# Performance work log

Measured on AMD Instinct MI355X. Metric: run time of the kernel, lower is better.

The kernel has to match this reference:

```python
import jax, jax.numpy as jnp
import numpy as np

B, L, H, HEADS = 4, 256, 256, 4
D = H // HEADS
NEG = jnp.float32(-2.0**32 + 1)


def setup_inputs() -> dict:
    key = jax.random.key(0)
    ks = jax.random.split(key, 16)
    inp = {
        "queries": jax.random.normal(ks[0], (B, L, H), jnp.float32),
        "keys": jax.random.normal(ks[1], (B, L, H), jnp.float32),
        "values": jax.random.normal(ks[2], (B, L, H), jnp.float32),
        "time_matrix_K": jax.random.normal(ks[3], (B, L, L, H), jnp.float32),
        "time_matrix_V": jax.random.normal(ks[4], (B, L, L, H), jnp.float32),
        "abs_pos_K": jax.random.normal(ks[5], (B, L, H), jnp.float32),
        "abs_pos_V": jax.random.normal(ks[6], (B, L, H), jnp.float32),
        "time_mask": jax.random.randint(ks[7], (B, L), 0, 2) == 1,
        "future_time_mask": jnp.triu(jnp.ones((L, L), bool), k=1),
        # linear layer params (torch Linear: y = x @ W.T + b)
        "Wq": jax.random.normal(ks[8], (H, H), jnp.float32) / np.sqrt(H),
        "bq": jax.random.normal(ks[9], (H,), jnp.float32) * 0.01,
        "Wk": jax.random.normal(ks[10], (H, H), jnp.float32) / np.sqrt(H),
        "bk": jax.random.normal(ks[11], (H,), jnp.float32) * 0.01,
        "Wv": jax.random.normal(ks[12], (H, H), jnp.float32) / np.sqrt(H),
        "bv": jax.random.normal(ks[13], (H,), jnp.float32) * 0.01,
    }
    return inp


def _split_heads(x):  # [B,L,H] -> [h,B,L,d]
    b, l, _ = x.shape
    return x.reshape(b, l, HEADS, D).transpose(2, 0, 1, 3)


def _split_heads_rel(t):  # [B,L,L,H] -> [h,B,L,L,d]
    b, l, _, _ = t.shape
    return t.reshape(b, l, l, HEADS, D).transpose(3, 0, 1, 2, 4)


def reference(queries, keys, values, time_matrix_K, time_matrix_V,
              abs_pos_K, abs_pos_V, time_mask, future_time_mask,
              Wq, bq, Wk, bk, Wv, bv):
    Q = _split_heads(queries @ Wq.T + bq)   # [h,B,L,d]
    K = _split_heads(keys @ Wk.T + bk)
    V = _split_heads(values @ Wv.T + bv)
    tK = _split_heads_rel(time_matrix_K)    # [h,B,L,L,d]
    tV = _split_heads_rel(time_matrix_V)
    pK = _split_heads(abs_pos_K)            # [h,B,L,d]
    pV = _split_heads(abs_pos_V)

    scores = jnp.einsum("hbqd,hbkd->hbqk", Q, K)
    scores += jnp.einsum("hbqd,hbkd->hbqk", Q, pK)
    scores += jnp.einsum("hbqkd,hbqd->hbqk", tK, Q)
    scores = scores / jnp.sqrt(jnp.float32(D))

    mask = time_mask[None, :, :, None] | future_time_mask[None, None, :, :]
    scores = jnp.where(mask, NEG, scores)
    attn = jax.nn.softmax(scores, axis=-1)  # [h,B,L,L]  (dropout: eval mode)

    out = jnp.einsum("hbqk,hbkd->hbqd", attn, V)
    out += jnp.einsum("hbqk,hbkd->hbqd", attn, pV)
    out += jnp.einsum("hbqk,hbqkd->hbqd", attn, tV)
    # merge heads: [h,B,L,d] -> [B,L,H]
    return out.transpose(1, 2, 0, 3).reshape(B, L, H)
```

## Files before the change

kernel.cpp:

```cpp
#include <hip/hip_runtime.h>
#include <math.h>
#include <stdint.h>

#define LSEQ 256
#define HD 256

typedef float floatx4 __attribute__((ext_vector_type(4)));

__device__ __forceinline__ float dot4(float4 a, float4 b) {
    return a.x * b.x + a.y * b.y + a.z * b.z + a.w * b.w;
}
__device__ __forceinline__ float4 add4(float4 a, float4 b) {
    return make_float4(a.x + b.x, a.y + b.y, a.z + b.z, a.w + b.w);
}
__device__ __forceinline__ float4 ldnt4(const float* p) {
    floatx4 r = __builtin_nontemporal_load((const floatx4*)p);
    return make_float4(r.x, r.y, r.z, r.w);
}

__global__ __launch_bounds__(256) void proj_kernel(
    const float* __restrict__ queries, const float* __restrict__ keys,
    const float* __restrict__ values,
    const float* __restrict__ apK, const float* __restrict__ apV,
    const float* __restrict__ Wq, const float* __restrict__ bq,
    const float* __restrict__ Wk, const float* __restrict__ bk,
    const float* __restrict__ Wv, const float* __restrict__ bv,
    float* __restrict__ Qo, float* __restrict__ Ko, float* __restrict__ Vo)
{
    const int R = 4;
    int tid = threadIdx.x;
    int row0 = blockIdx.x * R;

    float aq[R] = {0.f, 0.f, 0.f, 0.f};
    float ak[R] = {0.f, 0.f, 0.f, 0.f};
    float av[R] = {0.f, 0.f, 0.f, 0.f};

    const float* wq = Wq + tid * HD;
    const float* wk = Wk + tid * HD;
    const float* wv = Wv + tid * HD;

    #pragma unroll 2
    for (int i = 0; i < HD; i += 4) {
        float4 wq4 = *(const float4*)(wq + i);
        float4 wk4 = *(const float4*)(wk + i);
        float4 wv4 = *(const float4*)(wv + i);
        #pragma unroll
        for (int r = 0; r < R; ++r) {
            float4 xq = *(const float4*)(queries + (row0 + r) * HD + i);
            float4 xk = *(const float4*)(keys    + (row0 + r) * HD + i);
            float4 xv = *(const float4*)(values  + (row0 + r) * HD + i);
            aq[r] += dot4(xq, wq4);
            ak[r] += dot4(xk, wk4);
            av[r] += dot4(xv, wv4);
        }
    }
    #pragma unroll
    for (int r = 0; r < R; ++r) {
        int idx = (row0 + r) * HD + tid;
        Qo[idx] = aq[r] + bq[tid];
        Ko[idx] = ak[r] + bk[tid] + apK[idx];
        Vo[idx] = av[r] + bv[tid] + apV[idx];
    }
}

__global__ __launch_bounds__(256) void vmean_kernel(
    const float* __restrict__ Veff, float* __restrict__ Vm)
{
    int b = blockIdx.x;
    int t = threadIdx.x;
    const float* Vb = Veff + b * (LSEQ * HD);
    float s = 0.f;
    #pragma unroll 4
    for (int k = 0; k < LSEQ; ++k)
        s += Vb[k * HD + t];
    Vm[b * HD + t] = s * (1.0f / 256.0f);
}

__global__ __launch_bounds__(512) void attn_kernel(
    const float* __restrict__ Q, const float* __restrict__ Keff,
    const float* __restrict__ Veff, const float* __restrict__ tK,
    const float* __restrict__ tV, const float* __restrict__ Vm,
    const int* __restrict__ tmask, float* __restrict__ out)
{
    __shared__ float sc[4][260];
    __shared__ float outp[8][256];

    int bid = blockIdx.x;
    int q = 255 - (bid >> 2);
    int b = bid & 3;
    int bq = (b << 8) | q;

    int tid = threadIdx.x;
    int w = tid >> 6;
    int lane = tid & 63;
    int head = lane >> 4;
    int le4 = lane * 4;

    bool masked = tmask[bq] != 0;

    const float* tVr = tV + (size_t)bq * (LSEQ * HD);
    float4 acc = make_float4(0.f, 0.f, 0.f, 0.f);

    if (masked) {
        int r0 = w * 32;
        #pragma unroll 1
        for (int k = r0; k < r0 + 32; k += 8) {
            float4 t0 = ldnt4(tVr + (k    ) * HD + le4);
            float4 t1 = ldnt4(tVr + (k + 1) * HD + le4);
            float4 t2 = ldnt4(tVr + (k + 2) * HD + le4);
            float4 t3 = ldnt4(tVr + (k + 3) * HD + le4);
            float4 t4 = ldnt4(tVr + (k + 4) * HD + le4);
            float4 t5 = ldnt4(tVr + (k + 5) * HD + le4);
            float4 t6 = ldnt4(tVr + (k + 6) * HD + le4);
            float4 t7 = ldnt4(tVr + (k + 7) * HD + le4);
            acc.x += ((t0.x + t1.x) + (t2.x + t3.x)) + ((t4.x + t5.x) + (t6.x + t7.x));
            acc.y += ((t0.y + t1.y) + (t2.y + t3.y)) + ((t4.y + t5.y) + (t6.y + t7.y));
            acc.z += ((t0.z + t1.z) + (t2.z + t3.z)) + ((t4.z + t5.z) + (t6.z + t7.z));
            acc.w += ((t0.w + t1.w) + (t2.w + t3.w)) + ((t4.w + t5.w) + (t6.w + t7.w));
        }
    } else {
        const float* tKr = tK + (size_t)bq * (LSEQ * HD);
        const float* Kb  = Keff + b * (LSEQ * HD);
        const float* Vb  = Veff + b * (LSEQ * HD);
        float4 q4 = *(const float4*)(Q + bq * HD + le4);

        int nk = q + 1;
        int run = (nk + 7) >> 3;
        int r0 = w * run;
        int rend = min(r0 + run, nk);

        int k = r0;
        for (; k + 3 < rend; k += 4) {
            float4 t0 = ldnt4(tKr + (k    ) * HD + le4);
            float4 t1 = ldnt4(tKr + (k + 1) * HD + le4);
            float4 t2 = ldnt4(tKr + (k + 2) * HD + le4);
            float4 t3 = ldnt4(tKr + (k + 3) * HD + le4);
            float4 c0 = *(const float4*)(Kb + (k    ) * HD + le4);
            float4 c1 = *(const float4*)(Kb + (k + 1) * HD + le4);
            float4 c2 = *(const float4*)(Kb + (k + 2) * HD + le4);
            float4 c3 = *(const float4*)(Kb + (k + 3) * HD + le4);
            float s0 = dot4(q4, add4(t0, c0));
            float s1 = dot4(q4, add4(t1, c1));
            float s2 = dot4(q4, add4(t2, c2));
            float s3 = dot4(q4, add4(t3, c3));
            #pragma unroll
            for (int off = 1; off <= 8; off <<= 1) {
                s0 += __shfl_xor(s0, off);
                s1 += __shfl_xor(s1, off);
                s2 += __shfl_xor(s2, off);
                s3 += __shfl_xor(s3, off);
            }
            if ((lane & 15) == 0) {
                sc[head][k    ] = s0 * 0.125f;
                sc[head][k + 1] = s1 * 0.125f;
                sc[head][k + 2] = s2 * 0.125f;
                sc[head][k + 3] = s3 * 0.125f;
            }
        }
        for (; k < rend; ++k) {
            float4 t0 = ldnt4(tKr + k * HD + le4);
            float4 c0 = *(const float4*)(Kb + k * HD + le4);
            float s0 = dot4(q4, add4(t0, c0));
            #pragma unroll
            for (int off = 1; off <= 8; off <<= 1)
                s0 += __shfl_xor(s0, off);
            if ((lane & 15) == 0) sc[head][k] = s0 * 0.125f;
        }
        __syncthreads();

        if (w < 4) {
            int k0 = lane * 4;
            float4 vv = *(const float4*)(&sc[w][k0]);
            float x0 = (k0 + 0 <= q) ? vv.x : -INFINITY;
            float x1 = (k0 + 1 <= q) ? vv.y : -INFINITY;
            float x2 = (k0 + 2 <= q) ? vv.z : -INFINITY;
            float x3 = (k0 + 3 <= q) ? vv.w : -INFINITY;
            float m = fmaxf(fmaxf(x0, x1), fmaxf(x2, x3));
            #pragma unroll
            for (int off = 32; off >= 1; off >>= 1)
                m = fmaxf(m, __shfl_xor(m, off));
            float e0 = __expf(x0 - m);
            float e1 = __expf(x1 - m);
            float e2 = __expf(x2 - m);
            float e3 = __expf(x3 - m);
            float ssum = e0 + e1 + e2 + e3;
            #pragma unroll
            for (int off = 32; off >= 1; off >>= 1)
                ssum += __shfl_xor(ssum, off);
            float inv = 1.0f / ssum;
            *(float4*)(&sc[w][k0]) = make_float4(e0 * inv, e1 * inv,
                                                 e2 * inv, e3 * inv);
        }
        __syncthreads();

        k = r0;
        for (; k + 3 < rend; k += 4) {
            float4 t0 = ldnt4(tVr + (k    ) * HD + le4);
            float4 t1 = ldnt4(tVr + (k + 1) * HD + le4);
            float4 t2 = ldnt4(tVr + (k + 2) * HD + le4);
            float4 t3 = ldnt4(tVr + (k + 3) * HD + le4);
            float4 v0 = *(const float4*)(Vb + (k    ) * HD + le4);
            float4 v1 = *(const float4*)(Vb + (k + 1) * HD + le4);
            float4 v2 = *(const float4*)(Vb + (k + 2) * HD + le4);
            float4 v3 = *(const float4*)(Vb + (k + 3) * HD + le4);
            float a0 = sc[head][k    ];
            float a1 = sc[head][k + 1];
            float a2 = sc[head][k + 2];
            float a3 = sc[head][k + 3];
            acc.x += a0 * (t0.x + v0.x) + a1 * (t1.x + v1.x)
                   + a2 * (t2.x + v2.x) + a3 * (t3.x + v3.x);
            acc.y += a0 * (t0.y + v0.y) + a1 * (t1.y + v1.y)
                   + a2 * (t2.y + v2.y) + a3 * (t3.y + v3.y);
            acc.z += a0 * (t0.z + v0.z) + a1 * (t1.z + v1.z)
                   + a2 * (t2.z + v2.z) + a3 * (t3.z + v3.z);
            acc.w += a0 * (t0.w + v0.w) + a1 * (t1.w + v1.w)
                   + a2 * (t2.w + v2.w) + a3 * (t3.w + v3.w);
        }
        for (; k < rend; ++k) {
            float4 t0 = ldnt4(tVr + k * HD + le4);
            float4 v0 = *(const float4*)(Vb + k * HD + le4);
            float a0 = sc[head][k];
            acc.x += a0 * (t0.x + v0.x);
            acc.y += a0 * (t0.y + v0.y);
            acc.z += a0 * (t0.z + v0.z);
            acc.w += a0 * (t0.w + v0.w);
        }
    }

    *(float4*)(&outp[w][le4]) = acc;
    __syncthreads();
    if (tid < 256) {
        float o = 0.f;
        #pragma unroll
        for (int p = 0; p < 8; ++p) o += outp[p][tid];
        if (masked) o = o * (1.0f / 256.0f) + Vm[b * HD + tid];
        out[(size_t)bq * HD + tid] = o;
    }
}

extern "C" void kernel_launch(void* const* d_in, const int* in_sizes, int n_in,
                              void* d_out, int out_size, void* d_ws, size_t ws_size,
                              hipStream_t stream) {
    const float* queries = (const float*)d_in[0];
    const float* keys    = (const float*)d_in[1];
    const float* values  = (const float*)d_in[2];
    const float* tK      = (const float*)d_in[3];
    const float* tV      = (const float*)d_in[4];
    const float* apK     = (const float*)d_in[5];
    const float* apV     = (const float*)d_in[6];
    const int*   tmask   = (const int*)d_in[7];
    const float* Wq = (const float*)d_in[9];
    const float* bq = (const float*)d_in[10];
    const float* Wk = (const float*)d_in[11];
    const float* bk = (const float*)d_in[12];
    const float* Wv = (const float*)d_in[13];
    const float* bv = (const float*)d_in[14];

    float* ws = (float*)d_ws;
    float* Qo = ws;
    float* Ko = ws + 262144;
    float* Vo = ws + 524288;
    float* Vm = ws + 786432;
    float* out = (float*)d_out;

    proj_kernel<<<256, 256, 0, stream>>>(queries, keys, values, apK, apV,
                                         Wq, bq, Wk, bk, Wv, bv, Qo, Ko, Vo);
    vmean_kernel<<<4, 256, 0, stream>>>(Vo, Vm);
    attn_kernel<<<1024, 512, 0, stream>>>(Qo, Ko, Vo, tK, tV, Vm, tmask, out);
}
```

Before: 103.5 us.

## Software-pipeline attention row loads with double-buffered 8-row register batches

Replaces the 4-row unrolled score and value loops with a macro-driven double-buffered pipeline that loads 8 rows into one register set while consuming the previous set. The K and tK streams are split into separate passes, with an extra shared-memory buffer for the K partial scores, and likewise V and tV are accumulated in separate passes. Launch bounds now request 2 blocks per CU. The goal is more loads in flight to hide HBM latency on the large tK/tV streams, at the cost of more registers, extra LDS traffic and more shuffle reductions.

```diff
diff --git a/kernel.cpp b/kernel.cpp
--- a/kernel.cpp
+++ b/kernel.cpp
@@ -10,13 +10,74 @@
 __device__ __forceinline__ float dot4(float4 a, float4 b) {
     return a.x * b.x + a.y * b.y + a.z * b.z + a.w * b.w;
 }
-__device__ __forceinline__ float4 add4(float4 a, float4 b) {
-    return make_float4(a.x + b.x, a.y + b.y, a.z + b.z, a.w + b.w);
-}
 __device__ __forceinline__ float4 ldnt4(const float* p) {
     floatx4 r = __builtin_nontemporal_load((const floatx4*)p);
     return make_float4(r.x, r.y, r.z, r.w);
 }
+
+#define LOAD8NT(R, base, kk) do { _Pragma("unroll") \
+    for (int j = 0; j < 8; ++j) R[j] = ldnt4((base) + (size_t)((kk) + j) * HD + le4); } while (0)
+#define LOAD8P(R, base, kk) do { _Pragma("unroll") \
+    for (int j = 0; j < 8; ++j) R[j] = *(const float4*)((base) + (size_t)((kk) + j) * HD + le4); } while (0)
+
+#define CONS8_K1(R, kk) do { _Pragma("unroll") \
+    for (int j = 0; j < 8; ++j) { \
+        float s = dot4(q4, R[j]); \
+        s += __shfl_xor(s, 1); s += __shfl_xor(s, 2); \
+        s += __shfl_xor(s, 4); s += __shfl_xor(s, 8); \
+        if ((lane & 15) == 0) scK[head][(kk) + j] = s; } } while (0)
+#define CONS8_K2(R, kk) do { _Pragma("unroll") \
+    for (int j = 0; j < 8; ++j) { \
+        float s = dot4(q4, R[j]); \
+        s += __shfl_xor(s, 1); s += __shfl_xor(s, 2); \
+        s += __shfl_xor(s, 4); s += __shfl_xor(s, 8); \
+        if ((lane & 15) == 0) sc[head][(kk) + j] = (s + scK[head][(kk) + j]) * 0.125f; } } while (0)
+#define CONS8_V(R, kk) do { _Pragma("unroll") \
+    for (int j = 0; j < 8; ++j) { \
+        float a = sc[head][(kk) + j]; \
+        acc.x += a * R[j].x; acc.y += a * R[j].y; \
+        acc.z += a * R[j].z; acc.w += a * R[j].w; } } while (0)
+#define CONS8_S(R, kk) do { _Pragma("unroll") \
+    for (int j = 0; j < 8; ++j) { \
+        acc.x += R[j].x; acc.y += R[j].y; acc.z += R[j].z; acc.w += R[j].w; } } while (0)
+
+#define PIPE(LOADM, CONSM, CONS1, base, r0v, rendv) do { \
+    int n_ = (rendv) > (r0v) ? (rendv) - (r0v) : 0; \
+    int k_ = (r0v); \
+    float4 A_[8], B_[8]; \
+    if (n_ >= 8) { \
+        LOADM(A_, base, k_); \
+        if (n_ >= 16) { \
+            LOADM(B_, base, k_ + 8); CONSM(A_, k_); \
+            if (n_ >= 24) { \
+                LOADM(A_, base, k_ + 16); CONSM(B_, k_ + 8); \
+                if (n_ >= 32) { \
+                    LOADM(B_, base, k_ + 24); CONSM(A_, k_ + 16); CONSM(B_, k_ + 24); \
+                } else { CONSM(A_, k_ + 16); } \
+            } else { CONSM(B_, k_ + 8); } \
+        } else { CONSM(A_, k_); } \
+        k_ += (n_ & ~7); \
+    } \
+    for (int jj = 0; jj < (n_ & 7); ++jj, ++k_) { \
+        float4 T_ = *(const float4*)((base) + (size_t)k_ * HD + le4); \
+        CONS1(T_, k_); \
+    } } while (0)
+
+#define CONS1_K1(T, kk) do { \
+    float s = dot4(q4, T); \
+    s += __shfl_xor(s, 1); s += __shfl_xor(s, 2); \
+    s += __shfl_xor(s, 4); s += __shfl_xor(s, 8); \
+    if ((lane & 15) == 0) scK[head][kk] = s; } while (0)
+#define CONS1_K2(T, kk) do { \
+    float s = dot4(q4, T); \
+    s += __shfl_xor(s, 1); s += __shfl_xor(s, 2); \
+    s += __shfl_xor(s, 4); s += __shfl_xor(s, 8); \
+    if ((lane & 15) == 0) sc[head][kk] = (s + scK[head][kk]) * 0.125f; } while (0)
+#define CONS1_V(T, kk) do { \
+    float a = sc[head][kk]; \
+    acc.x += a * T.x; acc.y += a * T.y; acc.z += a * T.z; acc.w += a * T.w; } while (0)
+#define CONS1_S(T, kk) do { \
+    acc.x += T.x; acc.y += T.y; acc.z += T.z; acc.w += T.w; } while (0)
 
 __global__ __launch_bounds__(256) void proj_kernel(
     const float* __restrict__ queries, const float* __restrict__ keys,
@@ -76,12 +137,13 @@
     Vm[b * HD + t] = s * (1.0f / 256.0f);
 }
 
-__global__ __launch_bounds__(512) void attn_kernel(
+__global__ __launch_bounds__(512, 2) void attn_kernel(
     const float* __restrict__ Q, const float* __restrict__ Keff,
     const float* __restrict__ Veff, const float* __restrict__ tK,
     const float* __restrict__ tV, const float* __restrict__ Vm,
     const int* __restrict__ tmask, float* __restrict__ out)
 {
+    __shared__ float scK[4][260];
     __shared__ float sc[4][260];
     __shared__ float outp[8][256];
 
@@ -103,21 +165,7 @@
 
     if (masked) {
         int r0 = w * 32;
-        #pragma unroll 1
-        for (int k = r0; k < r0 + 32; k += 8) {
-            float4 t0 = ldnt4(tVr + (k    ) * HD + le4);
-            float4 t1 = ldnt4(tVr + (k + 1) * HD + le4);
-            float4 t2 = ldnt4(tVr + (k + 2) * HD + le4);
-            float4 t3 = ldnt4(tVr + (k + 3) * HD + le4);
-            float4 t4 = ldnt4(tVr + (k + 4) * HD + le4);
-            float4 t5 = ldnt4(tVr + (k + 5) * HD + le4);
-            float4 t6 = ldnt4(tVr + (k + 6) * HD + le4);
-            float4 t7 = ldnt4(tVr + (k + 7) * HD + le4);
-            acc.x += ((t0.x + t1.x) + (t2.x + t3.x)) + ((t4.x + t5.x) + (t6.x + t7.x));
-            acc.y += ((t0.y + t1.y) + (t2.y + t3.y)) + ((t4.y + t5.y) + (t6.y + t7.y));
-            acc.z += ((t0.z + t1.z) + (t2.z + t3.z)) + ((t4.z + t5.z) + (t6.z + t7.z));
-            acc.w += ((t0.w + t1.w) + (t2.w + t3.w)) + ((t4.w + t5.w) + (t6.w + t7.w));
-        }
+        PIPE(LOAD8NT, CONS8_S, CONS1_S, tVr, r0, r0 + 32);
     } else {
         const float* tKr = tK + (size_t)bq * (LSEQ * HD);
         const float* Kb  = Keff + b * (LSEQ * HD);
@@ -129,43 +177,8 @@
         int r0 = w * run;
         int rend = min(r0 + run, nk);
 
-        int k = r0;
-        for (; k + 3 < rend; k += 4) {
-            float4 t0 = ldnt4(tKr + (k    ) * HD + le4);
-            float4 t1 = ldnt4(tKr + (k + 1) * HD + le4);
-            float4 t2 = ldnt4(tKr + (k + 2) * HD + le4);
-            float4 t3 = ldnt4(tKr + (k + 3) * HD + le4);
-            float4 c0 = *(const float4*)(Kb + (k    ) * HD + le4);
-            float4 c1 = *(const float4*)(Kb + (k + 1) * HD + le4);
-            float4 c2 = *(const float4*)(Kb + (k + 2) * HD + le4);
-            float4 c3 = *(const float4*)(Kb + (k + 3) * HD + le4);
-            float s0 = dot4(q4, add4(t0, c0));
-            float s1 = dot4(q4, add4(t1, c1));
-            float s2 = dot4(q4, add4(t2, c2));
-            float s3 = dot4(q4, add4(t3, c3));
-            #pragma unroll
-            for (int off = 1; off <= 8; off <<= 1) {
-                s0 += __shfl_xor(s0, off);
-                s1 += __shfl_xor(s1, off);
-                s2 += __shfl_xor(s2, off);
-                s3 += __shfl_xor(s3, off);
-            }
-            if ((lane & 15) == 0) {
-                sc[head][k    ] = s0 * 0.125f;
-                sc[head][k + 1] = s1 * 0.125f;
-                sc[head][k + 2] = s2 * 0.125f;
-                sc[head][k + 3] = s3 * 0.125f;
-            }
-        }
-        for (; k < rend; ++k) {
-            float4 t0 = ldnt4(tKr + k * HD + le4);
-            float4 c0 = *(const float4*)(Kb + k * HD + le4);
-            float s0 = dot4(q4, add4(t0, c0));
-            #pragma unroll
-            for (int off = 1; off <= 8; off <<= 1)
-                s0 += __shfl_xor(s0, off);
-            if ((lane & 15) == 0) sc[head][k] = s0 * 0.125f;
-        }
+        PIPE(LOAD8P, CONS8_K1, CONS1_K1, Kb, r0, rend);
+        PIPE(LOAD8NT, CONS8_K2, CONS1_K2, tKr, r0, rend);
         __syncthreads();
 
         if (w < 4) {
@@ -193,38 +206,8 @@
         }
         __syncthreads();
 
-        k = r0;
-        for (; k + 3 < rend; k += 4) {
-            float4 t0 = ldnt4(tVr + (k    ) * HD + le4);
-            float4 t1 = ldnt4(tVr + (k + 1) * HD + le4);
-            float4 t2 = ldnt4(tVr + (k + 2) * HD + le4);
-            float4 t3 = ldnt4(tVr + (k + 3) * HD + le4);
-            float4 v0 = *(const float4*)(Vb + (k    ) * HD + le4);
-            float4 v1 = *(const float4*)(Vb + (k + 1) * HD + le4);
-            float4 v2 = *(const float4*)(Vb + (k + 2) * HD + le4);
-            float4 v3 = *(const float4*)(Vb + (k + 3) * HD + le4);
-            float a0 = sc[head][k    ];
-            float a1 = sc[head][k + 1];
-            float a2 = sc[head][k + 2];
-            float a3 = sc[head][k + 3];
-            acc.x += a0 * (t0.x + v0.x) + a1 * (t1.x + v1.x)
-                   + a2 * (t2.x + v2.x) + a3 * (t3.x + v3.x);
-            acc.y += a0 * (t0.y + v0.y) + a1 * (t1.y + v1.y)
-                   + a2 * (t2.y + v2.y) + a3 * (t3.y + v3.y);
-            acc.z += a0 * (t0.z + v0.z) + a1 * (t1.z + v1.z)
-                   + a2 * (t2.z + v2.z) + a3 * (t3.z + v3.z);
-            acc.w += a0 * (t0.w + v0.w) + a1 * (t1.w + v1.w)
-                   + a2 * (t2.w + v2.w) + a3 * (t3.w + v3.w);
-        }
-        for (; k < rend; ++k) {
-            float4 t0 = ldnt4(tVr + k * HD + le4);
-            float4 v0 = *(const float4*)(Vb + k * HD + le4);
-            float a0 = sc[head][k];
-            acc.x += a0 * (t0.x + v0.x);
-            acc.y += a0 * (t0.y + v0.y);
-            acc.z += a0 * (t0.z + v0.z);
-            acc.w += a0 * (t0.w + v0.w);
-        }
+        PIPE(LOAD8NT, CONS8_V, CONS1_V, tVr, r0, rend);
+        PIPE(LOAD8P, CONS8_V, CONS1_V, Vb, r0, rend);
     }
 
     *(float4*)(&outp[w][le4]) = acc;
```

After: 102.8 us, median of 3. No clear change (-0.7%).
